# Kernel optimization log

Measured on AMD Instinct MI355X. Metric: run time of the kernel, lower is better.

The kernel has to match this reference:

```python
import jax, jax.numpy as jnp
import numpy as np

# group boundaries (start with 0), ragged sizes cycling 16/32/48/64
_SIZES = np.tile(np.array([16, 32, 48, 64], dtype=np.int64), 16)  # 64 groups
GROUP = np.concatenate([[0], np.cumsum(_SIZES)])                   # [65]
SEG_IDS = np.repeat(np.arange(len(_SIZES)), _SIZES)                # [T=2560]
N_GROUPS = len(_SIZES)
D0 = 128  # also the attention scale (module divides by d0, NOT sqrt(d0))
B, T = 256, int(GROUP[-1])


def setup_inputs() -> dict:
    key = jax.random.key(0)
    k1, k2 = jax.random.split(key)
    s_i = jax.random.normal(k1, (B, D0), dtype=jnp.float32)
    theta_i = jax.random.normal(k2, (B, T, D0), dtype=jnp.float32)
    return {"s_i": s_i, "theta_i": theta_i}


def reference(s_i, theta_i):
    # Fused ragged attention over all groups: q_len == 1 per group.
    seg = jnp.asarray(SEG_IDS)                                   # [T]
    # scores u[b,t] = <s_i[b], theta_i[b,t]> / d0
    u = jnp.einsum('bd,btd->bt', s_i, theta_i) / D0              # [B,T]
    ut = u.T                                                     # [T,B] (segment ops over leading axis)
    m = jax.ops.segment_max(ut, seg, num_segments=N_GROUPS)      # [G,B]
    e = jnp.exp(ut - m[seg])                                     # [T,B]
    denom = jax.ops.segment_sum(e, seg, num_segments=N_GROUPS)   # [G,B]
    attn = e / denom[seg]                                        # [T,B] per-group softmax
    # out[b,g,d] = sum_{t in group g} attn[t,b] * theta_i[b,t,d]
    w = attn[:, :, None] * theta_i.transpose(1, 0, 2)            # [T,B,D]
    out = jax.ops.segment_sum(w, seg, num_segments=N_GROUPS)     # [G,B,D]
    return out.transpose(1, 0, 2)                                # [B,G,D]
```

## Files before the change

### kernel.cpp

```cpp
#include <hip/hip_runtime.h>
#include <math.h>

constexpr int D = 128;
constexpr int B = 256;
constexpr int T = 2560;
constexpr int G = 64;
constexpr int R = 8;

__global__ __launch_bounds__(256, 8) void ragged_attn_wave(
    const float* __restrict__ s_i,
    const float* __restrict__ theta,
    float* __restrict__ out)
{
    const int w    = threadIdx.x >> 6;
    const int lane = threadIdx.x & 63;
    const int q    = blockIdx.x & 15;
    const int b    = blockIdx.x >> 4;
    const int g    = q * 4 + w;
    const int gm   = g & 3;
    const int S    = 16 * (gm + 1);
    const int t0   = (g >> 2) * 160 + (gm * (gm + 1) / 2) * 16;

    __shared__ float tile[4][R * 128];
    __shared__ float u_sh[4][R];

    const int h = lane >> 5;
    const int c = lane & 31;

    const float4 s4 = ((const float4*)(s_i + (size_t)b * D))[c];
    const float4* theta4 = (const float4*)(theta + ((size_t)b * T + t0) * D);

    float m = -INFINITY, l = 0.0f;
    float acc0 = 0.0f, acc1 = 0.0f;
    const int nch = S >> 3;

    float4 rb[4];
    #pragma unroll
    for (int k = 0; k < 4; ++k)
        rb[k] = theta4[(size_t)(2 * k + h) * 32 + c];

    for (int ch = 0; ch < nch; ++ch) {
        float dt[4];
        #pragma unroll
        for (int k = 0; k < 4; ++k) {
            const float4 v = rb[k];
            ((float4*)&tile[w][(2 * k + h) * 128])[c] = v;
            dt[k] = v.x * s4.x + v.y * s4.y + v.z * s4.z + v.w * s4.w;
        }
        if (ch + 1 < nch) {
            #pragma unroll
            for (int k = 0; k < 4; ++k)
                rb[k] = theta4[(size_t)((ch + 1) * R + 2 * k + h) * 32 + c];
        }
        #pragma unroll
        for (int k = 0; k < 4; ++k) {
            #pragma unroll
            for (int msk = 16; msk >= 1; msk >>= 1)
                dt[k] += __shfl_xor(dt[k], msk);
        }
        if (c == 0) {
            #pragma unroll
            for (int k = 0; k < 4; ++k)
                u_sh[w][2 * k + h] = dt[k] * (1.0f / 128.0f);
        }
        float uu[R];
        float cm = -INFINITY;
        #pragma unroll
        for (int t = 0; t < R; ++t) {
            uu[t] = u_sh[w][t];
            cm = fmaxf(cm, uu[t]);
        }
        const float m_new = fmaxf(m, cm);
        const float alpha = __expf(m - m_new);
        acc0 *= alpha;
        acc1 *= alpha;
        float se = 0.0f;
        #pragma unroll
        for (int t = 0; t < R; ++t) {
            const float e = __expf(uu[t] - m_new);
            se += e;
            acc0 += e * tile[w][t * 128 + lane];
            acc1 += e * tile[w][t * 128 + 64 + lane];
        }
        l = l * alpha + se;
        m = m_new;
    }

    float* op = out + ((size_t)b * G + g) * D;
    const float inv_l = 1.0f / l;
    op[lane]      = acc0 * inv_l;
    op[lane + 64] = acc1 * inv_l;
}

extern "C" void kernel_launch(void* const* d_in, const int* in_sizes, int n_in,
                              void* d_out, int out_size, void* d_ws, size_t ws_size,
                              hipStream_t stream) {
    const float* s_i   = (const float*)d_in[0];
    const float* theta = (const float*)d_in[1];
    float* out = (float*)d_out;

    ragged_attn_wave<<<dim3(B * 16), 256, 0, stream>>>(s_i, theta, out);
}
```

Before: 448.1 us.

## Balance ragged groups by pairing short and long groups per wave

Each wave now handles two groups, one of 16 with one of 64 rows or 32 with 48, so every wave processes the same 80 rows (10 chunks). The flash-style state is reset and the output written at the group boundary. This removes the load imbalance where waves handling 16-row groups sit idle beside waves handling 64-row groups, and halves the grid size. The cost is fewer total waves in flight and a branch inside the chunk loop.

```diff
diff --git a/kernel.cpp b/kernel.cpp
--- a/kernel.cpp
+++ b/kernel.cpp
@@ -6,6 +6,7 @@
 constexpr int T = 2560;
 constexpr int G = 64;
 constexpr int R = 8;
+constexpr int NCH = 10;
 
 __global__ __launch_bounds__(256, 8) void ragged_attn_wave(
     const float* __restrict__ s_i,
@@ -14,12 +15,16 @@
 {
     const int w    = threadIdx.x >> 6;
     const int lane = threadIdx.x & 63;
-    const int q    = blockIdx.x & 15;
-    const int b    = blockIdx.x >> 4;
-    const int g    = q * 4 + w;
-    const int gm   = g & 3;
-    const int S    = 16 * (gm + 1);
-    const int t0   = (g >> 2) * 160 + (gm * (gm + 1) / 2) * 16;
+    const int b    = blockIdx.x >> 3;
+    const int q    = (blockIdx.x & 7) * 2 + (w >> 1);
+    const int p    = w & 1;
+
+    const int gmA  = p;
+    const int gmB  = 3 - p;
+    const int SA   = 16 * (gmA + 1);
+    const int nchA = SA >> 3;
+    const int baseA = q * 160 + (gmA * (gmA + 1) / 2) * 16;
+    const int baseB = q * 160 + (gmB * (gmB + 1) / 2) * 16;
 
     __shared__ float tile[4][R * 128];
     __shared__ float u_sh[4][R];
@@ -28,18 +33,24 @@
     const int c = lane & 31;
 
     const float4 s4 = ((const float4*)(s_i + (size_t)b * D))[c];
-    const float4* theta4 = (const float4*)(theta + ((size_t)b * T + t0) * D);
+    const float4* tbase = (const float4*)(theta + (size_t)b * T * D);
+
+    auto rowbase = [&](int ch) -> int {
+        return (ch < nchA) ? (baseA + ch * R) : (baseB + (ch - nchA) * R);
+    };
 
     float m = -INFINITY, l = 0.0f;
     float acc0 = 0.0f, acc1 = 0.0f;
-    const int nch = S >> 3;
 
     float4 rb[4];
-    #pragma unroll
-    for (int k = 0; k < 4; ++k)
-        rb[k] = theta4[(size_t)(2 * k + h) * 32 + c];
+    {
+        const int r0 = rowbase(0);
+        #pragma unroll
+        for (int k = 0; k < 4; ++k)
+            rb[k] = tbase[(size_t)(r0 + 2 * k + h) * 32 + c];
+    }
 
-    for (int ch = 0; ch < nch; ++ch) {
+    for (int ch = 0; ch < NCH; ++ch) {
         float dt[4];
         #pragma unroll
         for (int k = 0; k < 4; ++k) {
@@ -47,10 +58,11 @@
             ((float4*)&tile[w][(2 * k + h) * 128])[c] = v;
             dt[k] = v.x * s4.x + v.y * s4.y + v.z * s4.z + v.w * s4.w;
         }
-        if (ch + 1 < nch) {
+        if (ch + 1 < NCH) {
+            const int rn = rowbase(ch + 1);
             #pragma unroll
             for (int k = 0; k < 4; ++k)
-                rb[k] = theta4[(size_t)((ch + 1) * R + 2 * k + h) * 32 + c];
+                rb[k] = tbase[(size_t)(rn + 2 * k + h) * 32 + c];
         }
         #pragma unroll
         for (int k = 0; k < 4; ++k) {
@@ -84,12 +96,16 @@
         }
         l = l * alpha + se;
         m = m_new;
+
+        if (ch == nchA - 1 || ch == NCH - 1) {
+            const int gm = (ch == nchA - 1) ? gmA : gmB;
+            float* op = out + ((size_t)b * G + q * 4 + gm) * D;
+            const float inv_l = 1.0f / l;
+            op[lane]      = acc0 * inv_l;
+            op[lane + 64] = acc1 * inv_l;
+            m = -INFINITY; l = 0.0f; acc0 = 0.0f; acc1 = 0.0f;
+        }
     }
-
-    float* op = out + ((size_t)b * G + g) * D;
-    const float inv_l = 1.0f / l;
-    op[lane]      = acc0 * inv_l;
-    op[lane + 64] = acc1 * inv_l;
 }
 
 extern "C" void kernel_launch(void* const* d_in, const int* in_sizes, int n_in,
@@ -99,5 +115,5 @@
     const float* theta = (const float*)d_in[1];
     float* out = (float*)d_out;
 
-    ragged_attn_wave<<<dim3(B * 16), 256, 0, stream>>>(s_i, theta, out);
+    ragged_attn_wave<<<dim3(B * 8), 256, 0, stream>>>(s_i, theta, out);
 }
```

Measured after the change: 452.9 us. Within noise of the previous version (+1.1%).
